# Kernel optimization log

Measured on AMD Instinct MI355X. Metric: run time of the kernel, lower is better.

The kernel has to match this reference:

```python
import jax, jax.numpy as jnp
import numpy as np

LUT_K = 6
OUT_NUM = 1024
LUT_NUM = 64  # ceil(384 / 6)


def setup_inputs() -> dict:
    key = jax.random.key(0)
    k1, k2 = jax.random.split(key)
    x = jax.random.uniform(k1, (16, 2, OUT_NUM, LUT_NUM * LUT_K), dtype=jnp.float32)
    # learned LUT table parameter: [out_num, lut_num, 2**lut_k], randn like nn.Parameter init
    w = jax.random.normal(k2, (OUT_NUM, LUT_NUM, 1 << LUT_K), dtype=jnp.float32)
    return {"x": x, "w": w}


def reference(x, w):
    lut_k = LUT_K
    b, r, out_num, _ = x.shape
    _, lut_num, _ = w.shape
    # split input features into per-LUT k-bit groups: [b, r, out, lut_num, lut_k]
    xb = x.reshape(b, r, out_num, lut_num, lut_k)
    # soft binary quantization of w (hard=False, tau=1.0): (tanh(w) + 1) / 2
    w_q = (jnp.tanh(w) + 1.0) * 0.5
    # binary-tree LUT interpolation: start from the 2**k table split into pairs
    y = w_q.reshape(1, 1, out_num, lut_num, 1 << (lut_k - 1), 2)
    for level in range(lut_k):
        bit = xb[..., level][..., None]  # [b, r, out, lut_num, 1]
        y = (1.0 - bit) * y[..., 0] + bit * y[..., 1]
        if level < lut_k - 1:
            y = y.reshape(b, r, out_num, lut_num, 1 << (lut_k - level - 2), 2)
    # final y: [b, r, out_num, lut_num, 1] -> squeeze
    return jnp.squeeze(y, axis=-1)
```

## Files before the change

### kernel.cpp

```cpp
#include <hip/hip_runtime.h>
#include <math.h>

#define OUT_NUM 1024
#define LUT_NUM 64
#define LUT_K   6
#define TBL     64
#define WSTRIDE 65

__device__ __forceinline__ float softbit(float v) {
    return __builtin_amdgcn_rcpf(1.0f + __expf(-2.0f * v));
}

__global__ __launch_bounds__(256, 4)
void lut_fwd_kernel(const float* __restrict__ x,
                    const float* __restrict__ w,
                    float* __restrict__ out)
{
    __shared__ float wq[LUT_NUM * WSTRIDE];

    const int o = blockIdx.x;
    const int t = threadIdx.x;

    const float4* wrow4 = reinterpret_cast<const float4*>(w + (size_t)o * (LUT_NUM * TBL));
#pragma unroll
    for (int i = 0; i < 4; ++i) {
        const int f4 = t + 256 * i;
        const float4 v = wrow4[f4];
        const int f    = f4 * 4;
        const int lutc = f >> 6;
        const int p    = (f & 63) >> 1;
        const float s0 = softbit(v.x);
        const float s1 = softbit(v.y);
        const float s2 = softbit(v.z);
        const float s3 = softbit(v.w);
        float* row = &wq[lutc * WSTRIDE];
        row[p]          = s0;
        row[32 + p]     = s1 - s0;
        row[p + 1]      = s2;
        row[33 + p]     = s3 - s2;
    }
    __syncthreads();

    const int lut = t & 63;
    const int g   = t >> 6;

    const float* row = &wq[lut * WSTRIDE];
    float evn[32], dif[32];
#pragma unroll
    for (int p = 0; p < 32; ++p) { evn[p] = row[p]; dif[p] = row[32 + p]; }

    const float* xb = x + (size_t)o * (LUT_NUM * LUT_K) + lut * LUT_K;
    float* ob = out + (size_t)o * LUT_NUM + lut;

#pragma unroll
    for (int j = 0; j < 8; ++j) {
        const int br = g * 8 + j;
        const float2* xp = reinterpret_cast<const float2*>(xb + (size_t)br * (OUT_NUM * LUT_NUM * LUT_K));
        const float2 p01 = xp[0];
        const float2 p23 = xp[1];
        const float2 p45 = xp[2];

        float y[32];
#pragma unroll
        for (int p = 0; p < 32; ++p)
            y[p] = fmaf(p01.x, dif[p], evn[p]);
#pragma unroll
        for (int p = 0; p < 16; ++p)
            y[p] = fmaf(p01.y, y[2*p+1] - y[2*p], y[2*p]);
#pragma unroll
        for (int p = 0; p < 8; ++p)
            y[p] = fmaf(p23.x, y[2*p+1] - y[2*p], y[2*p]);
#pragma unroll
        for (int p = 0; p < 4; ++p)
            y[p] = fmaf(p23.y, y[2*p+1] - y[2*p], y[2*p]);
#pragma unroll
        for (int p = 0; p < 2; ++p)
            y[p] = fmaf(p45.x, y[2*p+1] - y[2*p], y[2*p]);
        const float res = fmaf(p45.y, y[1] - y[0], y[0]);

        ob[(size_t)br * (OUT_NUM * LUT_NUM)] = res;
    }
}

extern "C" void kernel_launch(void* const* d_in, const int* in_sizes, int n_in,
                              void* d_out, int out_size, void* d_ws, size_t ws_size,
                              hipStream_t stream)
{
    const float* x   = (const float*)d_in[0];
    const float* w   = (const float*)d_in[1];
    float*       out = (float*)d_out;
    lut_fwd_kernel<<<OUT_NUM, 256, 0, stream>>>(x, w, out);
}
```

Measured before the change: 93.61 us.

## Split each LUT interpolation across four lanes with shuffle-based final levels

Each LUT evaluation is now spread over four lanes, each holding an eighth of the table instead of all 64 entries. The last two tree levels are combined with xor shuffles, and the block grows to 512 threads covering 16 batch rows per row-group. This cuts per-thread registers and raises occupancy. In exchange the four lanes load the same x values redundantly, shuffles are added, and only one lane in four writes the result.

```diff
diff --git a/kernel.cpp b/kernel.cpp
--- a/kernel.cpp
+++ b/kernel.cpp
@@ -3,15 +3,16 @@
 
 #define OUT_NUM 1024
 #define LUT_NUM 64
-#define LUT_K   6
 #define TBL     64
-#define WSTRIDE 65
+#define WSTRIDE 68
+#define XROW    (LUT_NUM * 6)
+#define BR_TOT  32
 
 __device__ __forceinline__ float softbit(float v) {
     return __builtin_amdgcn_rcpf(1.0f + __expf(-2.0f * v));
 }
 
-__global__ __launch_bounds__(256, 4)
+__global__ __launch_bounds__(512, 8)
 void lut_fwd_kernel(const float* __restrict__ x,
                     const float* __restrict__ w,
                     float* __restrict__ out)
@@ -23,8 +24,8 @@
 
     const float4* wrow4 = reinterpret_cast<const float4*>(w + (size_t)o * (LUT_NUM * TBL));
 #pragma unroll
-    for (int i = 0; i < 4; ++i) {
-        const int f4 = t + 256 * i;
+    for (int i = 0; i < 2; ++i) {
+        const int f4 = t + 512 * i;
         const float4 v = wrow4[f4];
         const int f    = f4 * 4;
         const int lutc = f >> 6;
@@ -34,51 +35,57 @@
         const float s2 = softbit(v.z);
         const float s3 = softbit(v.w);
         float* row = &wq[lutc * WSTRIDE];
-        row[p]          = s0;
-        row[32 + p]     = s1 - s0;
-        row[p + 1]      = s2;
-        row[33 + p]     = s3 - s2;
+        row[p]      = s0;
+        row[32 + p] = s1 - s0;
+        row[p + 1]  = s2;
+        row[33 + p] = s3 - s2;
     }
     __syncthreads();
 
-    const int lut = t & 63;
-    const int g   = t >> 6;
+    const int h   = t & 3;
+    const int lut = (t >> 2) & 63;
+    const int rg  = t >> 8;
 
-    const float* row = &wq[lut * WSTRIDE];
-    float evn[32], dif[32];
+    const float* row = &wq[lut * WSTRIDE + 8 * h];
+    float evn[8], dif[8];
 #pragma unroll
-    for (int p = 0; p < 32; ++p) { evn[p] = row[p]; dif[p] = row[32 + p]; }
+    for (int i = 0; i < 8; ++i) { evn[i] = row[i]; dif[i] = row[32 + i]; }
 
-    const float* xb = x + (size_t)o * (LUT_NUM * LUT_K) + lut * LUT_K;
+    const float* xb = x + (size_t)o * XROW + lut * 6;
     float* ob = out + (size_t)o * LUT_NUM + lut;
+    const bool writer = (h == 0);
 
-#pragma unroll
-    for (int j = 0; j < 8; ++j) {
-        const int br = g * 8 + j;
-        const float2* xp = reinterpret_cast<const float2*>(xb + (size_t)br * (OUT_NUM * LUT_NUM * LUT_K));
+#pragma unroll 2
+    for (int j = 0; j < 16; ++j) {
+        const int br = rg * 16 + j;
+        const float2* xp = reinterpret_cast<const float2*>(xb + (size_t)br * (OUT_NUM * XROW));
         const float2 p01 = xp[0];
         const float2 p23 = xp[1];
         const float2 p45 = xp[2];
 
-        float y[32];
+        float z0[8];
 #pragma unroll
-        for (int p = 0; p < 32; ++p)
-            y[p] = fmaf(p01.x, dif[p], evn[p]);
+        for (int i = 0; i < 8; ++i) z0[i] = fmaf(p01.x, dif[i], evn[i]);
+        float z1[4];
 #pragma unroll
-        for (int p = 0; p < 16; ++p)
-            y[p] = fmaf(p01.y, y[2*p+1] - y[2*p], y[2*p]);
+        for (int i = 0; i < 4; ++i) z1[i] = fmaf(p01.y, z0[2*i+1] - z0[2*i], z0[2*i]);
+        float z2[2];
 #pragma unroll
-        for (int p = 0; p < 8; ++p)
-            y[p] = fmaf(p23.x, y[2*p+1] - y[2*p], y[2*p]);
-#pragma unroll
-        for (int p = 0; p < 4; ++p)
-            y[p] = fmaf(p23.y, y[2*p+1] - y[2*p], y[2*p]);
-#pragma unroll
-        for (int p = 0; p < 2; ++p)
-            y[p] = fmaf(p45.x, y[2*p+1] - y[2*p], y[2*p]);
-        const float res = fmaf(p45.y, y[1] - y[0], y[0]);
+        for (int i = 0; i < 2; ++i) z2[i] = fmaf(p23.x, z1[2*i+1] - z1[2*i], z1[2*i]);
+        float z = fmaf(p23.y, z2[1] - z2[0], z2[0]);
 
-        ob[(size_t)br * (OUT_NUM * LUT_NUM)] = res;
+        float pt = __shfl_xor(z, 1);
+        float lo = (h & 1) ? pt : z;
+        float hi = (h & 1) ? z  : pt;
+        z = fmaf(p45.x, hi - lo, lo);
+
+        pt = __shfl_xor(z, 2);
+        lo = (h & 2) ? pt : z;
+        hi = (h & 2) ? z  : pt;
+        z = fmaf(p45.y, hi - lo, lo);
+
+        if (writer)
+            ob[(size_t)br * (OUT_NUM * LUT_NUM)] = z;
     }
 }
 
@@ -89,5 +96,5 @@
     const float* x   = (const float*)d_in[0];
     const float* w   = (const float*)d_in[1];
     float*       out = (float*)d_out;
-    lut_fwd_kernel<<<OUT_NUM, 256, 0, stream>>>(x, w, out);
+    lut_fwd_kernel<<<OUT_NUM, 512, 0, stream>>>(x, w, out);
 }
```

Result: slower. 103.4 us (+10.5%).

## Use 512-thread blocks with interleaved float2 LDS table read per row

Applied to the files above, without the earlier changes.

Doubles the block size to 512 threads so each thread handles 4 batch-rows instead of 8, and stores the quantized table as interleaved (even, diff) float2 pairs with stride 33. Instead of caching 64 table values in registers, each thread reads them from LDS for every row, with the row loop left un-unrolled. This aims to cut register pressure and raise occupancy and memory-level parallelism, at the cost of repeated LDS reads and less load batching per thread.

```diff
diff --git a/kernel.cpp b/kernel.cpp
--- a/kernel.cpp
+++ b/kernel.cpp
@@ -3,67 +3,63 @@
 
 #define OUT_NUM 1024
 #define LUT_NUM 64
-#define LUT_K   6
 #define TBL     64
-#define WSTRIDE 65
+#define XROW    (LUT_NUM * 6)
+#define LSTRIDE 33
 
 __device__ __forceinline__ float softbit(float v) {
     return __builtin_amdgcn_rcpf(1.0f + __expf(-2.0f * v));
 }
 
-__global__ __launch_bounds__(256, 4)
+__global__ __launch_bounds__(512, 8)
 void lut_fwd_kernel(const float* __restrict__ x,
                     const float* __restrict__ w,
                     float* __restrict__ out)
 {
-    __shared__ float wq[LUT_NUM * WSTRIDE];
+    __shared__ float2 wq[LUT_NUM * LSTRIDE];
 
     const int o = blockIdx.x;
     const int t = threadIdx.x;
 
     const float4* wrow4 = reinterpret_cast<const float4*>(w + (size_t)o * (LUT_NUM * TBL));
 #pragma unroll
-    for (int i = 0; i < 4; ++i) {
-        const int f4 = t + 256 * i;
+    for (int i = 0; i < 2; ++i) {
+        const int f4   = t + 512 * i;
         const float4 v = wrow4[f4];
-        const int f    = f4 * 4;
-        const int lutc = f >> 6;
-        const int p    = (f & 63) >> 1;
+        const int lutc = f4 >> 4;
+        const int m    = f4 & 15;
         const float s0 = softbit(v.x);
         const float s1 = softbit(v.y);
         const float s2 = softbit(v.z);
         const float s3 = softbit(v.w);
-        float* row = &wq[lutc * WSTRIDE];
-        row[p]          = s0;
-        row[32 + p]     = s1 - s0;
-        row[p + 1]      = s2;
-        row[33 + p]     = s3 - s2;
+        float2* row = &wq[lutc * LSTRIDE];
+        row[2*m]     = make_float2(s0, s1 - s0);
+        row[2*m + 1] = make_float2(s2, s3 - s2);
     }
     __syncthreads();
 
     const int lut = t & 63;
-    const int g   = t >> 6;
+    const int rg  = t >> 6;
+    const float2* row = &wq[lut * LSTRIDE];
 
-    const float* row = &wq[lut * WSTRIDE];
-    float evn[32], dif[32];
-#pragma unroll
-    for (int p = 0; p < 32; ++p) { evn[p] = row[p]; dif[p] = row[32 + p]; }
-
-    const float* xb = x + (size_t)o * (LUT_NUM * LUT_K) + lut * LUT_K;
+    const float* xb = x + (size_t)o * XROW + lut * 6;
     float* ob = out + (size_t)o * LUT_NUM + lut;
 
-#pragma unroll
-    for (int j = 0; j < 8; ++j) {
-        const int br = g * 8 + j;
-        const float2* xp = reinterpret_cast<const float2*>(xb + (size_t)br * (OUT_NUM * LUT_NUM * LUT_K));
+#pragma unroll 1
+    for (int j = 0; j < 4; ++j) {
+        const int br = rg * 4 + j;
+        const float2* xp = reinterpret_cast<const float2*>(
+            xb + (size_t)br * (OUT_NUM * XROW));
         const float2 p01 = xp[0];
         const float2 p23 = xp[1];
         const float2 p45 = xp[2];
 
         float y[32];
 #pragma unroll
-        for (int p = 0; p < 32; ++p)
-            y[p] = fmaf(p01.x, dif[p], evn[p]);
+        for (int p = 0; p < 32; ++p) {
+            const float2 ed = row[p];
+            y[p] = fmaf(p01.x, ed.y, ed.x);
+        }
 #pragma unroll
         for (int p = 0; p < 16; ++p)
             y[p] = fmaf(p01.y, y[2*p+1] - y[2*p], y[2*p]);
@@ -89,5 +85,5 @@
     const float* x   = (const float*)d_in[0];
     const float* w   = (const float*)d_in[1];
     float*       out = (float*)d_out;
-    lut_fwd_kernel<<<OUT_NUM, 256, 0, stream>>>(x, w, out);
+    lut_fwd_kernel<<<OUT_NUM, 512, 0, stream>>>(x, w, out);
 }
```

After: 248.9 us. +165.9%, slower.

## Stage x through double-buffered shared memory with coalesced float4 loads

Applied to the files above, without the earlier changes.

Replaces the per-thread strided float2 loads of x with coalesced float4 global loads of whole rows into a double-buffered LDS buffer. The loads for the next batch are prefetched into registers while the current batch is computed. The weight table stride is padded to 68 so table rows can be read as float4. This targets the uncoalesced 24-byte-per-thread access pattern, at the cost of extra barriers and LDS traffic, and the smaller grid work per block may limit the achievable overlap.

```diff
diff --git a/kernel.cpp b/kernel.cpp
--- a/kernel.cpp
+++ b/kernel.cpp
@@ -3,9 +3,10 @@
 
 #define OUT_NUM 1024
 #define LUT_NUM 64
-#define LUT_K   6
 #define TBL     64
-#define WSTRIDE 65
+#define XROWD   384
+#define WSTRIDE 68
+#define BUFD    3072
 
 __device__ __forceinline__ float softbit(float v) {
     return __builtin_amdgcn_rcpf(1.0f + __expf(-2.0f * v));
@@ -16,69 +17,115 @@
                     const float* __restrict__ w,
                     float* __restrict__ out)
 {
-    __shared__ float wq[LUT_NUM * WSTRIDE];
+    __shared__ __align__(16) float smem[2 * BUFD];
 
     const int o = blockIdx.x;
     const int t = threadIdx.x;
 
-    const float4* wrow4 = reinterpret_cast<const float4*>(w + (size_t)o * (LUT_NUM * TBL));
+    {
+        float* wq = smem;
+        const float4* wrow4 = reinterpret_cast<const float4*>(w + (size_t)o * (LUT_NUM * TBL));
 #pragma unroll
-    for (int i = 0; i < 4; ++i) {
-        const int f4 = t + 256 * i;
-        const float4 v = wrow4[f4];
-        const int f    = f4 * 4;
-        const int lutc = f >> 6;
-        const int p    = (f & 63) >> 1;
-        const float s0 = softbit(v.x);
-        const float s1 = softbit(v.y);
-        const float s2 = softbit(v.z);
-        const float s3 = softbit(v.w);
-        float* row = &wq[lutc * WSTRIDE];
-        row[p]          = s0;
-        row[32 + p]     = s1 - s0;
-        row[p + 1]      = s2;
-        row[33 + p]     = s3 - s2;
+        for (int i = 0; i < 4; ++i) {
+            const int f4   = t + 256 * i;
+            const float4 v = wrow4[f4];
+            const int lutc = f4 >> 4;
+            const int m    = f4 & 15;
+            const float s0 = softbit(v.x);
+            const float s1 = softbit(v.y);
+            const float s2 = softbit(v.z);
+            const float s3 = softbit(v.w);
+            float* row = &wq[lutc * WSTRIDE];
+            row[2*m]      = s0;
+            row[32 + 2*m] = s1 - s0;
+            row[2*m + 1]  = s2;
+            row[33 + 2*m] = s3 - s2;
+        }
     }
     __syncthreads();
 
     const int lut = t & 63;
-    const int g   = t >> 6;
+    const int r0  = t >> 6;
 
-    const float* row = &wq[lut * WSTRIDE];
     float evn[32], dif[32];
+    {
+        const float4* rv = reinterpret_cast<const float4*>(&smem[lut * WSTRIDE]);
 #pragma unroll
-    for (int p = 0; p < 32; ++p) { evn[p] = row[p]; dif[p] = row[32 + p]; }
+        for (int q = 0; q < 8; ++q) {
+            const float4 e = rv[q];
+            const float4 d = rv[8 + q];
+            evn[4*q] = e.x; evn[4*q+1] = e.y; evn[4*q+2] = e.z; evn[4*q+3] = e.w;
+            dif[4*q] = d.x; dif[4*q+1] = d.y; dif[4*q+2] = d.z; dif[4*q+3] = d.w;
+        }
+    }
+    __syncthreads();
 
-    const float* xb = x + (size_t)o * (LUT_NUM * LUT_K) + lut * LUT_K;
+    const float4* xg4   = reinterpret_cast<const float4*>(x);
+    float4*       xbuf4 = reinterpret_cast<float4*>(smem);
+
+#pragma unroll
+    for (int i = 0; i < 3; ++i) {
+        const int f = t + 256 * i;
+        const int k = f / 96;
+        const int c = f - 96 * k;
+        xbuf4[f] = xg4[((size_t)k * OUT_NUM + o) * 96 + c];
+    }
+    __syncthreads();
+
     float* ob = out + (size_t)o * LUT_NUM + lut;
 
+#pragma unroll 1
+    for (int b = 0; b < 4; ++b) {
+        float4 nf0, nf1, nf2;
+        if (b < 3) {
 #pragma unroll
-    for (int j = 0; j < 8; ++j) {
-        const int br = g * 8 + j;
-        const float2* xp = reinterpret_cast<const float2*>(xb + (size_t)br * (OUT_NUM * LUT_NUM * LUT_K));
-        const float2 p01 = xp[0];
-        const float2 p23 = xp[1];
-        const float2 p45 = xp[2];
+            for (int i = 0; i < 3; ++i) {
+                const int f = t + 256 * i;
+                const int k = f / 96;
+                const int c = f - 96 * k;
+                const float4 v = xg4[((size_t)(8*(b+1) + k) * OUT_NUM + o) * 96 + c];
+                if (i == 0) nf0 = v; else if (i == 1) nf1 = v; else nf2 = v;
+            }
+        }
 
-        float y[32];
+        const float* cb = smem + (b & 1) * BUFD;
 #pragma unroll
-        for (int p = 0; p < 32; ++p)
-            y[p] = fmaf(p01.x, dif[p], evn[p]);
+        for (int s = 0; s < 2; ++s) {
+            const int r  = r0 + 4 * s;
+            const int br = 8 * b + r;
+            const float2* xp = reinterpret_cast<const float2*>(cb + r * XROWD + lut * 6);
+            const float2 p01 = xp[0];
+            const float2 p23 = xp[1];
+            const float2 p45 = xp[2];
+
+            float y[32];
 #pragma unroll
-        for (int p = 0; p < 16; ++p)
-            y[p] = fmaf(p01.y, y[2*p+1] - y[2*p], y[2*p]);
+            for (int p = 0; p < 32; ++p)
+                y[p] = fmaf(p01.x, dif[p], evn[p]);
 #pragma unroll
-        for (int p = 0; p < 8; ++p)
-            y[p] = fmaf(p23.x, y[2*p+1] - y[2*p], y[2*p]);
+            for (int p = 0; p < 16; ++p)
+                y[p] = fmaf(p01.y, y[2*p+1] - y[2*p], y[2*p]);
 #pragma unroll
-        for (int p = 0; p < 4; ++p)
-            y[p] = fmaf(p23.y, y[2*p+1] - y[2*p], y[2*p]);
+            for (int p = 0; p < 8; ++p)
+                y[p] = fmaf(p23.x, y[2*p+1] - y[2*p], y[2*p]);
 #pragma unroll
-        for (int p = 0; p < 2; ++p)
-            y[p] = fmaf(p45.x, y[2*p+1] - y[2*p], y[2*p]);
-        const float res = fmaf(p45.y, y[1] - y[0], y[0]);
+            for (int p = 0; p < 4; ++p)
+                y[p] = fmaf(p23.y, y[2*p+1] - y[2*p], y[2*p]);
+#pragma unroll
+            for (int p = 0; p < 2; ++p)
+                y[p] = fmaf(p45.x, y[2*p+1] - y[2*p], y[2*p]);
+            const float res = fmaf(p45.y, y[1] - y[0], y[0]);
 
-        ob[(size_t)br * (OUT_NUM * LUT_NUM)] = res;
+            ob[(size_t)br * (OUT_NUM * LUT_NUM)] = res;
+        }
+
+        if (b < 3) {
+            float4* nb = xbuf4 + ((b + 1) & 1) * (BUFD / 4);
+            nb[t]       = nf0;
+            nb[t + 256] = nf1;
+            nb[t + 512] = nf2;
+        }
+        __syncthreads();
     }
 }
 
```

Measured after the change: 92.94 us. Within noise of the previous version (-0.7%).
